# Kernel tuning notes

Hardware: AMD Instinct MI355X
Metric: run time of the kernel (lower is better)

Reference implementation:

```python
import jax, jax.numpy as jnp
import numpy as np

BITS = 4
OFF = 8          # 2**(BITS-1)
QLEVELS = 15.0   # 2**BITS - 1
IN_F, OUT_F, FP_F, TOKENS = 4096, 4096, 256, 4096
INT_F = IN_F - FP_F


def unpack_i4(w_packed):
    """Invert pack_to_i4: packed uint8 col k holds signed int4 cols (2k: low nibble, 2k+1: high)."""
    lo = (w_packed & 0x0F).astype(jnp.int8)
    hi = ((w_packed >> 4) & 0x0F).astype(jnp.int8)
    lo = jnp.where(lo >= 8, lo - 16, lo)
    hi = jnp.where(hi >= 8, hi - 16, hi)
    return jnp.stack([lo, hi], axis=-1).reshape(w_packed.shape[0], -1)  # (out, int_features)


def setup_inputs() -> dict:
    key = jax.random.key(0)
    k1, k2, k3, k4, k5 = jax.random.split(key, 5)
    x = jax.random.normal(k1, (1, TOKENS, IN_F), dtype=jnp.float16)
    perm = jax.random.permutation(k2, IN_F)
    fp_indices = jnp.sort(perm[:FP_F]).astype(jnp.int64)
    int_indices = jnp.sort(perm[FP_F:]).astype(jnp.int64)
    # signed int4 weight values in [-8, 7], packed two-per-byte like pack_to_i4
    w_vals = jax.random.randint(k3, (OUT_F, INT_F), -8, 8, dtype=jnp.int8)
    u = (w_vals.astype(jnp.int32) & 0x0F).astype(jnp.uint8)
    int_weight = (u[:, 0::2] | (u[:, 1::2] << 4)).astype(jnp.uint8)  # (out, INT_F//2)
    weights_scales = (jax.random.uniform(k4, (OUT_F, 1)) * 0.01 + 1e-3).astype(jnp.float16)
    # reduced_w = row-sum of the dequantized int-column weights (as in from_float)
    reduced_w = (w_vals.astype(jnp.float32).sum(axis=1, keepdims=True)
                 * weights_scales.astype(jnp.float32)).T.astype(jnp.float16)  # (1, out)
    fp_weight = (jax.random.normal(k5, (OUT_F, FP_F)) * 0.02).astype(jnp.float16)
    bias = jnp.zeros((OUT_F,), dtype=jnp.float16)
    return {"x": x, "int_weight": int_weight, "weights_scales": weights_scales,
            "reduced_w": reduced_w, "fp_weight": fp_weight, "bias": bias,
            "int_indices": int_indices, "fp_indices": fp_indices}


def reference(x, int_weight, weights_scales, reduced_w, fp_weight, bias,
              int_indices, fp_indices):
    x2 = x[0]                                   # (M, in_features)
    int_x = x2[:, int_indices].astype(jnp.float32)   # (M, INT_F)
    fp_x = x2[:, fp_indices].astype(jnp.float32)     # (M, FP_F)
    # asymmetric per-row quantization to signed int4
    mn = int_x.min(axis=1, keepdims=True)
    mx = int_x.max(axis=1, keepdims=True)
    scale = jnp.maximum((mx - mn) / QLEVELS, 1e-8)   # (M,1)
    zero = mn                                        # (M,1)
    q = jnp.clip(jnp.round((int_x - zero) / scale) - OFF, -8, 7).astype(jnp.int8)
    w_int = unpack_i4(int_weight)                    # (out, INT_F) int8
    int_result = jnp.matmul(q.astype(jnp.int32), w_int.T.astype(jnp.int32))  # (M, out) int32
    fp_result = fp_x @ fp_weight.T.astype(jnp.float32) + bias.astype(jnp.float32)
    # asym dequant: x ~ (q + OFF)*scale + zero, W = w_int * w_scale, sum_j W_j = reduced_w
    w_scale = weights_scales.astype(jnp.float32)[:, 0][None, :]   # (1, out)
    out = (scale * w_scale * int_result.astype(jnp.float32)
           + (zero + scale * OFF) * reduced_w.astype(jnp.float32)
           + fp_result)
    return out.astype(jnp.float16)[None]             # (1, M, out)
```

## Files before the change

kernel.cpp:

```cpp
#include <hip/hip_runtime.h>
#include <hip/hip_bf16.h>

#define IN_FEAT 4096
#define OUT_FEAT 4096
#define FP_FEAT 256
#define INT_FEAT 3840
#define TOKENS 4096
#define PACKED_W (INT_FEAT / 2)

#define NT_I8 60
#define NT_ALL 68

typedef __attribute__((ext_vector_type(8))) short short8;
typedef __attribute__((ext_vector_type(4))) float f32x4;
typedef __attribute__((ext_vector_type(4))) int   int32x4;

#define AQ8_OFF   0u
#define WB8_OFF   16777216u
#define AFP_OFF   33554432u
#define WFP_OFF   35651584u
#define SCALE_OFF 37748736u
#define ZERO_OFF  37765120u
#define WS_NEED   37781504u

__global__ __launch_bounds__(256) void prep_kernel(
    const float* __restrict__ x,
    const int* __restrict__ int_idx_raw,
    const int* __restrict__ fp_idx_raw,
    const int* __restrict__ wpacked_raw,
    const float* __restrict__ fpw,
    const float* __restrict__ wscale,
    signed char* __restrict__ Aq8,
    __hip_bfloat16* __restrict__ Afp,
    signed char* __restrict__ Wb8,
    __hip_bfloat16* __restrict__ Wfp,
    float* __restrict__ scale_ws,
    float* __restrict__ zero_ws)
{
    const int t = threadIdx.x;
    if (blockIdx.x < TOKENS) {
        const int m = blockIdx.x;
        const float* xr = x + (size_t)m * IN_FEAT;
        const bool is64 = (int_idx_raw[1] == 0) && (int_idx_raw[3] == 0);

        float v[15];
        float mn = 1e30f, mx = -1e30f;
#pragma unroll
        for (int j = 0; j < 15; ++j) {
            int k = t + j * 256;
            int idx = is64 ? int_idx_raw[2 * k] : int_idx_raw[k];
            float f = xr[idx];
            v[j] = f;
            mn = fminf(mn, f);
            mx = fmaxf(mx, f);
        }
#pragma unroll
        for (int off = 1; off < 64; off <<= 1) {
            mn = fminf(mn, __shfl_xor(mn, off));
            mx = fmaxf(mx, __shfl_xor(mx, off));
        }
        __shared__ float smn[4], smx[4];
        int wid = t >> 6, lane = t & 63;
        if (lane == 0) { smn[wid] = mn; smx[wid] = mx; }
        __syncthreads();
        if (t == 0) {
            float rmn = fminf(fminf(smn[0], smn[1]), fminf(smn[2], smn[3]));
            float rmx = fmaxf(fmaxf(smx[0], smx[1]), fmaxf(smx[2], smx[3]));
            float sc = fmaxf((rmx - rmn) / 15.0f, 1e-8f);
            smn[0] = rmn;
            smx[0] = sc;
            scale_ws[m] = sc;
            zero_ws[m] = rmn;
        }
        __syncthreads();
        const float zero = smn[0];
        const float sc = smx[0];

        signed char* ar = Aq8 + (size_t)m * INT_FEAT;
#pragma unroll
        for (int j = 0; j < 15; ++j) {
            int k = t + j * 256;
            float q = rintf((v[j] - zero) / sc) - 8.0f;
            q = fminf(fmaxf(q, -8.0f), 7.0f);
            ar[k] = (signed char)(int)q;
        }
        int fpi = is64 ? fp_idx_raw[2 * t] : fp_idx_raw[t];
        Afp[(size_t)m * FP_FEAT + t] = __float2bfloat16(xr[fpi] / sc);
    } else {
        const int n = blockIdx.x - TOKENS;
        bool is_i32 = true;
#pragma unroll
        for (int j = 0; j < 8; ++j) {
            unsigned w = (unsigned)wpacked_raw[j];
            if (w > 0xFFu) is_i32 = false;
        }
        short* wo = (short*)(Wb8 + (size_t)n * INT_FEAT);
#pragma unroll
        for (int j = 0; j < 8; ++j) {
            int k = t + j * 256;
            if (k < PACKED_W) {
                int p = is_i32 ? wpacked_raw[(size_t)n * PACKED_W + k]
                               : ((const unsigned char*)wpacked_raw)[(size_t)n * PACKED_W + k];
                int lo = p & 15; if (lo >= 8) lo -= 16;
                int hi = (p >> 4) & 15; if (hi >= 8) hi -= 16;
                wo[k] = (short)(((unsigned char)lo) | ((unsigned short)(unsigned char)hi << 8));
            }
        }
        float wsn = wscale[n];
        Wfp[(size_t)n * FP_FEAT + t] = __float2bfloat16(fpw[(size_t)n * FP_FEAT + t] / wsn);
    }
}


__global__ __launch_bounds__(512, 2) void gemm256_i8(
    const signed char* __restrict__ Aq8,
    const __hip_bfloat16* __restrict__ Afp,
    const signed char* __restrict__ Wb8,
    const __hip_bfloat16* __restrict__ Wfp,
    const float* __restrict__ scale_ws,
    const float* __restrict__ zero_ws,
    const float* __restrict__ wscale,
    const float* __restrict__ reduced,
    const float* __restrict__ bias,
    float* __restrict__ out)
{
    __shared__ __align__(16) char lds[131072];

    const int t = threadIdx.x;
    const int lane = t & 63, wid = t >> 6;
    const int wr = wid >> 2;
    const int wc = wid & 3;
    const int r16 = lane & 15;
    const int kg = lane >> 4;

    const int bid = blockIdx.x;
    const int sb = (bid & 7) * 32 + (bid >> 3);
    const int tileM = (sb >> 4) * 256;
    const int tileN = (sb & 15) * 256;

    const int id0 = t, id1 = 512 + t;
    const int r0 = id0 >> 2, c0 = id0 & 3;
    const int r1 = id1 >> 2, c1 = id1 & 3;
    const int sw0 = ((c0 ^ ((r0 >> 1) & 3)) << 4);
    const int sw1 = ((c1 ^ ((r1 >> 1) & 3)) << 4);
    const char* a8_0 = (const char*)Aq8 + (size_t)(tileM + r0) * INT_FEAT + sw0;
    const char* a8_1 = (const char*)Aq8 + (size_t)(tileM + r1) * INT_FEAT + sw1;
    const char* b8_0 = (const char*)Wb8 + (size_t)(tileN + r0) * INT_FEAT + sw0;
    const char* b8_1 = (const char*)Wb8 + (size_t)(tileN + r1) * INT_FEAT + sw1;
    const char* af_0 = (const char*)Afp + (size_t)(tileM + r0) * 512 + sw0;
    const char* af_1 = (const char*)Afp + (size_t)(tileM + r1) * 512 + sw1;
    const char* bf_0 = (const char*)Wfp + (size_t)(tileN + r0) * 512 + sw0;
    const char* bf_1 = (const char*)Wfp + (size_t)(tileN + r1) * 512 + sw1;
    const int dst0 = id0 << 4, dst1 = id1 << 4;

    auto stage = [&](int vt, int bufB) {
        const bool i8p = vt < NT_I8;
        const int ko = i8p ? vt * 64 : (vt - NT_I8) * 64;
        const char* pa0 = (i8p ? a8_0 : af_0) + ko;
        const char* pa1 = (i8p ? a8_1 : af_1) + ko;
        const char* pb0 = (i8p ? b8_0 : bf_0) + ko;
        const char* pb1 = (i8p ? b8_1 : bf_1) + ko;
        __builtin_amdgcn_global_load_lds(
            (const __attribute__((address_space(1))) void*)pa0,
            (__attribute__((address_space(3))) void*)(lds + bufB + dst0), 16, 0, 0);
        __builtin_amdgcn_global_load_lds(
            (const __attribute__((address_space(1))) void*)pa1,
            (__attribute__((address_space(3))) void*)(lds + bufB + dst1), 16, 0, 0);
        __builtin_amdgcn_global_load_lds(
            (const __attribute__((address_space(1))) void*)pb0,
            (__attribute__((address_space(3))) void*)(lds + bufB + 16384 + dst0), 16, 0, 0);
        __builtin_amdgcn_global_load_lds(
            (const __attribute__((address_space(1))) void*)pb1,
            (__attribute__((address_space(3))) void*)(lds + bufB + 16384 + dst1), 16, 0, 0);
    };

    int aOff[8], bOff[4];
#pragma unroll
    for (int mf = 0; mf < 8; ++mf) {
        int ra = wr * 128 + mf * 16 + r16;
        aOff[mf] = ra * 64 + ((((ra >> 1) & 3) ^ kg) << 4);
    }
#pragma unroll
    for (int nf = 0; nf < 4; ++nf) {
        int rb = wc * 64 + nf * 16 + r16;
        bOff[nf] = 16384 + rb * 64 + ((((rb >> 1) & 3) ^ kg) << 4);
    }

    int32x4 acc[8][4];
#pragma unroll
    for (int mf = 0; mf < 8; ++mf)
#pragma unroll
        for (int nf = 0; nf < 4; ++nf)
            acc[mf][nf] = (int32x4){0, 0, 0, 0};

    stage(0, 0);
    stage(1, 32768);
    stage(2, 65536);
    asm volatile("s_waitcnt vmcnt(8)" ::: "memory");
    __builtin_amdgcn_sched_barrier(0);
    __builtin_amdgcn_s_barrier();

    for (int vt = 0; vt < NT_I8; ++vt) {
        const int bufB = (vt & 3) << 15;
        int32x4 bI[4], aI[8];
#pragma unroll
        for (int nf = 0; nf < 4; ++nf)
            bI[nf] = *(const int32x4*)(lds + bufB + bOff[nf]);
#pragma unroll
        for (int mf = 0; mf < 8; ++mf)
            aI[mf] = *(const int32x4*)(lds + bufB + aOff[mf]);

        stage(vt + 3, ((vt + 3) & 3) << 15);

#pragma unroll
        for (int mf = 0; mf < 8; ++mf)
#pragma unroll
            for (int nf = 0; nf < 4; ++nf)
                acc[mf][nf] = __builtin_amdgcn_mfma_i32_16x16x64_i8(
                    aI[mf], bI[nf], acc[mf][nf], 0, 0, 0);

        asm volatile("s_waitcnt vmcnt(8)" ::: "memory");
        __builtin_amdgcn_sched_barrier(0);
        __builtin_amdgcn_s_barrier();
    }

#pragma unroll
    for (int mf = 0; mf < 8; ++mf)
#pragma unroll
        for (int nf = 0; nf < 4; ++nf) {
            int32x4 vi = acc[mf][nf];
            f32x4 vf;
#pragma unroll
            for (int i = 0; i < 4; ++i) vf[i] = (float)vi[i];
            acc[mf][nf] = __builtin_bit_cast(int32x4, vf);
        }

    for (int vt = NT_I8; vt < NT_ALL; ++vt) {
        const int bufB = (vt & 3) << 15;
        short8 bF[4], aF[8];
#pragma unroll
        for (int nf = 0; nf < 4; ++nf)
            bF[nf] = *(const short8*)(lds + bufB + bOff[nf]);
#pragma unroll
        for (int mf = 0; mf < 8; ++mf)
            aF[mf] = *(const short8*)(lds + bufB + aOff[mf]);

        if (vt + 3 < NT_ALL)
            stage(vt + 3, ((vt + 3) & 3) << 15);

#pragma unroll
        for (int mf = 0; mf < 8; ++mf)
#pragma unroll
            for (int nf = 0; nf < 4; ++nf)
                acc[mf][nf] = __builtin_bit_cast(int32x4,
                    __builtin_amdgcn_mfma_f32_16x16x32_bf16(
                        aF[mf], bF[nf],
                        __builtin_bit_cast(f32x4, acc[mf][nf]), 0, 0, 0));

        if (vt <= NT_ALL - 4)
            asm volatile("s_waitcnt vmcnt(8)" ::: "memory");
        else if (vt == NT_ALL - 3)
            asm volatile("s_waitcnt vmcnt(4)" ::: "memory");
        else if (vt == NT_ALL - 2)
            asm volatile("s_waitcnt vmcnt(0)" ::: "memory");
        __builtin_amdgcn_sched_barrier(0);
        __builtin_amdgcn_s_barrier();
    }

    const int cr4 = kg * 4;
#pragma unroll
    for (int mf = 0; mf < 8; ++mf) {
#pragma unroll
        for (int nf = 0; nf < 4; ++nf) {
            int n = tileN + wc * 64 + nf * 16 + r16;
            float ws = wscale[n];
            float rd = reduced[n];
            float bs = bias[n];
            f32x4 av = __builtin_bit_cast(f32x4, acc[mf][nf]);
#pragma unroll
            for (int i = 0; i < 4; ++i) {
                int m = tileM + wr * 128 + mf * 16 + cr4 + i;
                float sc = scale_ws[m];
                float zr = zero_ws[m];
                out[(size_t)m * OUT_FEAT + n] =
                    sc * ws * av[i]
                    + (zr + sc * 8.0f) * rd + bs;
            }
        }
    }
}

extern "C" void kernel_launch(void* const* d_in, const int* in_sizes, int n_in,
                              void* d_out, int out_size, void* d_ws, size_t ws_size,
                              hipStream_t stream)
{
    const void* px = 0; const void* pw = 0; const void* pfpw = 0;
    const void* pii = 0; const void* pfi = 0;
    const void* p4096[3] = {0, 0, 0}; int n4096 = 0;
    for (int i = 0; i < n_in; ++i) {
        switch (in_sizes[i]) {
            case 16777216: px = d_in[i]; break;
            case 7864320:  pw = d_in[i]; break;
            case 1048576:  pfpw = d_in[i]; break;
            case 3840:     pii = d_in[i]; break;
            case 256:      pfi = d_in[i]; break;
            case 4096:     if (n4096 < 3) p4096[n4096++] = d_in[i]; break;
            default: break;
        }
    }
    if (!px || !pw || !pfpw || !pii || !pfi || n4096 != 3) return;

    const float* x       = (const float*)px;
    const int*   wpacked = (const int*)pw;
    const float* wscale  = (const float*)p4096[0];
    const float* reduced = (const float*)p4096[1];
    const float* bias    = (const float*)p4096[2];
    const float* fpw     = (const float*)pfpw;
    const int*   int_idx = (const int*)pii;
    const int*   fp_idx  = (const int*)pfi;
    float*       out     = (float*)d_out;

    if (ws_size < (size_t)WS_NEED) return;

    char* ws = (char*)d_ws;
    signed char*    Aq8 = (signed char*)(ws + AQ8_OFF);
    signed char*    Wb8 = (signed char*)(ws + WB8_OFF);
    __hip_bfloat16* Afp = (__hip_bfloat16*)(ws + AFP_OFF);
    __hip_bfloat16* Wfp = (__hip_bfloat16*)(ws + WFP_OFF);
    float* scale_ws     = (float*)(ws + SCALE_OFF);
    float* zero_ws      = (float*)(ws + ZERO_OFF);

    prep_kernel<<<TOKENS + OUT_FEAT, 256, 0, stream>>>(
        x, int_idx, fp_idx, wpacked, fpw, wscale,
        Aq8, Afp, Wb8, Wfp, scale_ws, zero_ws);
    gemm256_i8<<<256, 512, 0, stream>>>(Aq8, Afp, Wb8, Wfp,
                                        scale_ws, zero_ws,
                                        wscale, reduced, bias, out);
}
```

Before: 98.18 us.

## Double-buffer LDS fragment reads in registers across GEMM k-tiles

Restructures the main int8 and bf16 MFMA loops so that the LDS-to-register fragment loads for tile vt+1 are issued before the MFMAs of tile vt. Two register sets are used in ping-pong fashion, and the loop is unrolled by two with an explicit tail. The global-load wait tightens from vmcnt(8) to vmcnt(4), so one fewer stage is outstanding when crossing a barrier. The goal is to hide LDS read latency behind MFMA work. The cost is extra VGPR pressure, with 24 more int32x4 registers live at launch bounds 512,2, which risks spills.

```diff
diff --git a/kernel.cpp b/kernel.cpp
--- a/kernel.cpp
+++ b/kernel.cpp
@@ -111,6 +111,53 @@
     }
 }
 
+
+#define PREFETCH(VT, AN, BN)                                                   \
+    {                                                                          \
+        const int pbB = ((VT) & 3) << 15;                                      \
+        _Pragma("unroll")                                                      \
+        for (int nf = 0; nf < 4; ++nf)                                         \
+            BN[nf] = *(const int32x4*)(lds + pbB + bOff[nf]);                  \
+        _Pragma("unroll")                                                      \
+        for (int mf = 0; mf < 8; ++mf)                                         \
+            AN[mf] = *(const int32x4*)(lds + pbB + aOff[mf]);                  \
+    }
+
+#define MFMA_I8(AC, BC)                                                        \
+    _Pragma("unroll")                                                          \
+    for (int mf = 0; mf < 8; ++mf)                                             \
+        _Pragma("unroll")                                                      \
+        for (int nf = 0; nf < 4; ++nf)                                         \
+            acc[mf][nf] = __builtin_amdgcn_mfma_i32_16x16x64_i8(               \
+                AC[mf], BC[nf], acc[mf][nf], 0, 0, 0);
+
+#define MFMA_BF(AC, BC)                                                        \
+    _Pragma("unroll")                                                          \
+    for (int mf = 0; mf < 8; ++mf)                                             \
+        _Pragma("unroll")                                                      \
+        for (int nf = 0; nf < 4; ++nf)                                         \
+            acc[mf][nf] = __builtin_bit_cast(int32x4,                          \
+                __builtin_amdgcn_mfma_f32_16x16x32_bf16(                       \
+                    __builtin_bit_cast(short8, AC[mf]),                        \
+                    __builtin_bit_cast(short8, BC[nf]),                        \
+                    __builtin_bit_cast(f32x4, acc[mf][nf]), 0, 0, 0));
+
+#define ENDBAR4()                                                              \
+    asm volatile("s_waitcnt vmcnt(4)" ::: "memory");                           \
+    __builtin_amdgcn_sched_barrier(0);                                         \
+    __builtin_amdgcn_s_barrier();                                              \
+    __builtin_amdgcn_sched_barrier(0);
+
+#define ENDBAR0()                                                              \
+    asm volatile("s_waitcnt vmcnt(0)" ::: "memory");                           \
+    __builtin_amdgcn_sched_barrier(0);                                         \
+    __builtin_amdgcn_s_barrier();                                              \
+    __builtin_amdgcn_sched_barrier(0);
+
+#define ENDBARN()                                                              \
+    __builtin_amdgcn_sched_barrier(0);                                         \
+    __builtin_amdgcn_s_barrier();                                              \
+    __builtin_amdgcn_sched_barrier(0);
 
 __global__ __launch_bounds__(512, 2) void gemm256_i8(
     const signed char* __restrict__ Aq8,
@@ -193,36 +240,38 @@
         for (int nf = 0; nf < 4; ++nf)
             acc[mf][nf] = (int32x4){0, 0, 0, 0};
 
+    int32x4 aP[8], bP[4], aN[8], bN[4];
+
     stage(0, 0);
     stage(1, 32768);
     stage(2, 65536);
-    asm volatile("s_waitcnt vmcnt(8)" ::: "memory");
+    asm volatile("s_waitcnt vmcnt(4)" ::: "memory");
     __builtin_amdgcn_sched_barrier(0);
     __builtin_amdgcn_s_barrier();
-
-    for (int vt = 0; vt < NT_I8; ++vt) {
-        const int bufB = (vt & 3) << 15;
-        int32x4 bI[4], aI[8];
-#pragma unroll
-        for (int nf = 0; nf < 4; ++nf)
-            bI[nf] = *(const int32x4*)(lds + bufB + bOff[nf]);
-#pragma unroll
-        for (int mf = 0; mf < 8; ++mf)
-            aI[mf] = *(const int32x4*)(lds + bufB + aOff[mf]);
-
+    __builtin_amdgcn_sched_barrier(0);
+    PREFETCH(0, aP, bP);
+
+    for (int vt = 0; vt < NT_I8 - 2; vt += 2) {
+        PREFETCH(vt + 1, aN, bN);
         stage(vt + 3, ((vt + 3) & 3) << 15);
-
-#pragma unroll
-        for (int mf = 0; mf < 8; ++mf)
-#pragma unroll
-            for (int nf = 0; nf < 4; ++nf)
-                acc[mf][nf] = __builtin_amdgcn_mfma_i32_16x16x64_i8(
-                    aI[mf], bI[nf], acc[mf][nf], 0, 0, 0);
-
-        asm volatile("s_waitcnt vmcnt(8)" ::: "memory");
-        __builtin_amdgcn_sched_barrier(0);
-        __builtin_amdgcn_s_barrier();
-    }
+        MFMA_I8(aP, bP);
+        ENDBAR4();
+
+        PREFETCH(vt + 2, aP, bP);
+        stage(vt + 4, ((vt + 4) & 3) << 15);
+        MFMA_I8(aN, bN);
+        ENDBAR4();
+    }
+
+    PREFETCH(59, aN, bN);
+    stage(61, (61 & 3) << 15);
+    MFMA_I8(aP, bP);
+    ENDBAR4();
+
+    PREFETCH(60, aP, bP);
+    stage(62, (62 & 3) << 15);
+    MFMA_I8(aN, bN);
+    ENDBAR4();
 
 #pragma unroll
     for (int mf = 0; mf < 8; ++mf)
@@ -235,37 +284,14 @@
             acc[mf][nf] = __builtin_bit_cast(int32x4, vf);
         }
 
-    for (int vt = NT_I8; vt < NT_ALL; ++vt) {
-        const int bufB = (vt & 3) << 15;
-        short8 bF[4], aF[8];
-#pragma unroll
-        for (int nf = 0; nf < 4; ++nf)
-            bF[nf] = *(const short8*)(lds + bufB + bOff[nf]);
-#pragma unroll
-        for (int mf = 0; mf < 8; ++mf)
-            aF[mf] = *(const short8*)(lds + bufB + aOff[mf]);
-
-        if (vt + 3 < NT_ALL)
-            stage(vt + 3, ((vt + 3) & 3) << 15);
-
-#pragma unroll
-        for (int mf = 0; mf < 8; ++mf)
-#pragma unroll
-            for (int nf = 0; nf < 4; ++nf)
-                acc[mf][nf] = __builtin_bit_cast(int32x4,
-                    __builtin_amdgcn_mfma_f32_16x16x32_bf16(
-                        aF[mf], bF[nf],
-                        __builtin_bit_cast(f32x4, acc[mf][nf]), 0, 0, 0));
-
-        if (vt <= NT_ALL - 4)
-            asm volatile("s_waitcnt vmcnt(8)" ::: "memory");
-        else if (vt == NT_ALL - 3)
-            asm volatile("s_waitcnt vmcnt(4)" ::: "memory");
-        else if (vt == NT_ALL - 2)
-            asm volatile("s_waitcnt vmcnt(0)" ::: "memory");
-        __builtin_amdgcn_sched_barrier(0);
-        __builtin_amdgcn_s_barrier();
-    }
+    PREFETCH(61, aN, bN); stage(63, (63 & 3) << 15); MFMA_BF(aP, bP); ENDBAR4();
+    PREFETCH(62, aP, bP); stage(64, (64 & 3) << 15); MFMA_BF(aN, bN); ENDBAR4();
+    PREFETCH(63, aN, bN); stage(65, (65 & 3) << 15); MFMA_BF(aP, bP); ENDBAR4();
+    PREFETCH(64, aP, bP); stage(66, (66 & 3) << 15); MFMA_BF(aN, bN); ENDBAR4();
+    PREFETCH(65, aN, bN); stage(67, (67 & 3) << 15); MFMA_BF(aP, bP); ENDBAR4();
+    PREFETCH(66, aP, bP);                            MFMA_BF(aN, bN); ENDBAR0();
+    PREFETCH(67, aN, bN);                            MFMA_BF(aP, bP); ENDBARN();
+    MFMA_BF(aN, bN);
 
     const int cr4 = kg * 4;
 #pragma unroll
```

After: 96.53 us (median of 2 runs). Within noise of the previous version (-1.7%).
